# Kernel optimization log

Measured on AMD Instinct MI355X. Metric: run time of the kernel, lower is better.

The kernel has to match this reference:

```python
import jax, jax.numpy as jnp
import numpy as np

TEMPERATURE = 0.07
SIM_THRESHOLD = 0.5


def setup_inputs() -> dict:
    key = jax.random.key(0)
    k1, k2 = jax.random.split(key)
    features = jax.random.normal(k1, (4096, 2, 128), dtype=jnp.float32)
    labels = jax.random.randint(k2, (4096, 100), 0, 2).astype(jnp.float32)
    return {"features": features, "labels": labels}


def reference(features, labels):
    B, V, D = features.shape

    # label Jaccard similarity -> positive/negative masks [B, B]
    intersection = labels @ labels.T
    row_sum = jnp.sum(labels, axis=1, keepdims=True)
    union = row_sum + row_sum.T - intersection
    similarity = intersection / (union + 1e-6)
    positive_mask = (similarity >= SIM_THRESHOLD).astype(jnp.float32)
    negative_mask = 1.0 - positive_mask

    # torch.cat(torch.unbind(features, dim=1), dim=0) -> [V*B, D] (view-major)
    contrast_feature = jnp.transpose(features, (1, 0, 2)).reshape(V * B, D)
    dot_similarities = (contrast_feature @ contrast_feature.T) / TEMPERATURE  # [VB, VB]

    # numerical stability: subtract detached row max over the FULL row
    logits_max = jax.lax.stop_gradient(jnp.max(dot_similarities, axis=1, keepdims=True))
    logits = dot_similarities - logits_max

    # only the top-left [B, B] block is ever indexed by the original loop
    e = jnp.exp(logits[:B, :B])
    pos_sum = jnp.sum(e * positive_mask, axis=1)  # [B]
    neg_sum = jnp.sum(e * negative_mask, axis=1)  # [B]

    has_pos = jnp.sum(positive_mask, axis=1) > 0  # rows with >=1 positive
    pos_safe = jnp.where(has_pos, pos_sum, 1.0)
    den_safe = jnp.where(has_pos, pos_sum + neg_sum, 1.0)
    per_row = -jnp.log(pos_safe / den_safe)

    count = jnp.sum(has_pos.astype(jnp.float32))
    loss = jnp.sum(jnp.where(has_pos, per_row, 0.0)) / jnp.maximum(count, 1.0)
    return loss
```

## Files before the change

### kernel.cpp

```cpp
#include <hip/hip_runtime.h>
#include <math.h>

#define B_ROWS 4096
#define LBL 100
#define NCT 32
#define NTRI 528

typedef __attribute__((ext_vector_type(8))) short bf16x8;
typedef __attribute__((ext_vector_type(4))) float f32x4;

__device__ __forceinline__ unsigned f2bf(float x) {
  union { float f; unsigned u; } a; a.f = x;
  unsigned r = a.u + 0x7fffu + ((a.u >> 16) & 1u);
  return r >> 16;
}
__device__ __forceinline__ float bf2f(unsigned h) {
  return __uint_as_float(h << 16);
}

__global__ void prep_kernel(const float* __restrict__ feat,
                            const float* __restrict__ labels,
                            uint4* __restrict__ cf,
                            uint4* __restrict__ Lb,
                            int* __restrict__ rsv,
                            float* __restrict__ seedRaw,
                            float2* __restrict__ rowAcc,
                            unsigned* __restrict__ counter) {
  if (blockIdx.x == 0 && threadIdx.x == 0) *counter = 0u;
  int w = blockIdx.x * 4 + (threadIdx.x >> 6);
  int lane = threadIdx.x & 63;
  float2 f = ((const float2*)(feat + (size_t)w * 256))[lane];
  unsigned u0 = f2bf(f.x), u1 = f2bf(f.y);
  unsigned myu = u0 | (u1 << 16);
  float b0 = bf2f(u0), b1 = bf2f(u1);
  float s = b0 * b0 + b1 * b1;
  #pragma unroll
  for (int o = 32; o >= 1; o >>= 1) s += __shfl_xor(s, o);
  float x0 = labels[(size_t)w * LBL + lane];
  float x1 = (lane < LBL - 64) ? labels[(size_t)w * LBL + 64 + lane] : 0.0f;
  unsigned long long m0 = __ballot(x0 != 0.0f);
  unsigned long long m1 = __ballot(x1 != 0.0f);
  int kc = lane & 15;
  unsigned q0 = __shfl(myu, kc * 4 + 0);
  unsigned q1 = __shfl(myu, kc * 4 + 1);
  unsigned q2 = __shfl(myu, kc * 4 + 2);
  unsigned q3 = __shfl(myu, kc * 4 + 3);
  if (lane < 16)
    cf[(size_t)(w >> 7) * 2048 + kc * 128 + ((w & 127) ^ kc)] =
        make_uint4(q0, q1, q2, q3);
  if (lane == 0) {
    Lb[w] = make_uint4((unsigned)m0, (unsigned)(m0 >> 32),
                       (unsigned)m1, (unsigned)(m1 >> 32));
    rsv[w] = __popcll(m0) + __popcll(m1);
    seedRaw[w] = s - 0.15f;
    rowAcc[w] = make_float2(0.0f, 0.0f);
  }
}

__launch_bounds__(256, 1)
__global__ void main_kernel(const uint4* __restrict__ cf,
                            const uint4* __restrict__ Lb,
                            const int* __restrict__ rsv,
                            const float* __restrict__ seedRaw,
                            float2* __restrict__ rowAcc,
                            unsigned* __restrict__ counter,
                            float* __restrict__ out) {
  __shared__ unsigned s_done;
  __shared__ float s_p[4], s_c[4];

  int bid = blockIdx.x;
  int bx = 0, off = 0;
  while (bid >= off + (NCT - bx)) { off += NCT - bx; ++bx; }
  int by = bx + (bid - off);
  const bool diag = (bx == by);

  const int tid = threadIdx.x;
  const int lane = tid & 63;
  const int l15 = lane & 15;
  const int quad = lane >> 4;
  const int wave = tid >> 6;
  const int wi = (wave & 1) * 64;
  const int wj = (wave >> 1) * 64;
  const int rowBase = bx * 128;
  const int colBase = by * 128;
  const float invT = 1.0f / 0.07f;

  const uint4* Ab = cf + (size_t)bx * 2048;
  const uint4* Bb = cf + (size_t)by * 2048;

  f32x4 acc[4][4];
  #pragma unroll
  for (int ti = 0; ti < 4; ++ti)
    #pragma unroll
    for (int tj = 0; tj < 4; ++tj)
      acc[ti][tj] = (f32x4){0.f, 0.f, 0.f, 0.f};

  bf16x8 af[4], bfr[4], af2[4], bfr2[4];
  {
    const int kc = quad;
    #pragma unroll
    for (int t = 0; t < 4; ++t) {
      af[t]  = *(const bf16x8*)&Ab[kc * 128 + ((wi + t * 16 + l15) ^ kc)];
      bfr[t] = *(const bf16x8*)&Bb[kc * 128 + ((wj + t * 16 + l15) ^ kc)];
    }
  }
  #pragma unroll
  for (int ks = 0; ks < 4; ++ks) {
    if (ks < 3) {
      const int kc = (ks + 1) * 4 + quad;
      #pragma unroll
      for (int t = 0; t < 4; ++t) {
        af2[t]  = *(const bf16x8*)&Ab[kc * 128 + ((wi + t * 16 + l15) ^ kc)];
        bfr2[t] = *(const bf16x8*)&Bb[kc * 128 + ((wj + t * 16 + l15) ^ kc)];
      }
    }
    #pragma unroll
    for (int ti = 0; ti < 4; ++ti)
      #pragma unroll
      for (int tj = 0; tj < 4; ++tj)
        acc[ti][tj] = __builtin_amdgcn_mfma_f32_16x16x32_bf16(
            af[ti], bfr[tj], acc[ti][tj], 0, 0, 0);
    if (ks < 3) {
      #pragma unroll
      for (int t = 0; t < 4; ++t) { af[t] = af2[t]; bfr[t] = bfr2[t]; }
    }
  }

  uint4 clb[4];
  int crs[4];
  float scol[4], srow[16];
  #pragma unroll
  for (int tj = 0; tj < 4; ++tj) {
    int gcol = colBase + wj + tj * 16 + l15;
    clb[tj] = Lb[gcol];
    crs[tj] = rsv[gcol];
    scol[tj] = seedRaw[gcol];
  }
  #pragma unroll
  for (int ti = 0; ti < 4; ++ti) {
    float4 s4 = *(const float4*)&seedRaw[rowBase + wi + ti * 16 + quad * 4];
    srow[ti * 4 + 0] = s4.x; srow[ti * 4 + 1] = s4.y;
    srow[ti * 4 + 2] = s4.z; srow[ti * 4 + 3] = s4.w;
  }

  float p_s[16], n_s[16], cp[4], cn[4], cmax[4];
  #pragma unroll
  for (int i = 0; i < 16; ++i) { p_s[i] = 0.f; n_s[i] = 0.f; }
  #pragma unroll
  for (int tj = 0; tj < 4; ++tj) { cp[tj] = 0.f; cn[tj] = 0.f; cmax[tj] = -1e30f; }

  #pragma unroll
  for (int ti = 0; ti < 4; ++ti)
    #pragma unroll
    for (int r = 0; r < 4; ++r) {
      int si = ti * 4 + r;
      float l0 = acc[ti][0][r], l1 = acc[ti][1][r];
      float l2 = acc[ti][2][r], l3 = acc[ti][3][r];
      cmax[0] = fmaxf(cmax[0], l0);
      cmax[1] = fmaxf(cmax[1], l1);
      cmax[2] = fmaxf(cmax[2], l2);
      cmax[3] = fmaxf(cmax[3], l3);
      float tm = fmaxf(fmaxf(l0, l1), fmaxf(l2, l3));
      if (tm > srow[si] - 6.3f) {
        int grow = rowBase + wi + ti * 16 + quad * 4 + r;
        uint4 la = Lb[grow];
        int ra = rsv[grow];
        float p = p_s[si], n = n_s[si];
        float lv[4] = {l0, l1, l2, l3};
        #pragma unroll
        for (int tj = 0; tj < 4; ++tj) {
          float e = __expf((lv[tj] - srow[si]) * invT);
          int inter = __popc(la.x & clb[tj].x) + __popc(la.y & clb[tj].y) +
                      __popc(la.z & clb[tj].z) + __popc(la.w & clb[tj].w);
          if (3 * inter > ra + crs[tj]) p += e; else n += e;
        }
        p_s[si] = p;
        n_s[si] = n;
      }
    }

  if (!diag) {
    #pragma unroll
    for (int tj = 0; tj < 4; ++tj) {
      if (cmax[tj] > scol[tj] - 6.3f) {
        float p = cp[tj], n = cn[tj];
        #pragma unroll
        for (int ti = 0; ti < 4; ++ti)
          #pragma unroll
          for (int r = 0; r < 4; ++r) {
            float e = __expf((acc[ti][tj][r] - scol[tj]) * invT);
            int grow = rowBase + wi + ti * 16 + quad * 4 + r;
            uint4 la = Lb[grow];
            int inter = __popc(la.x & clb[tj].x) + __popc(la.y & clb[tj].y) +
                        __popc(la.z & clb[tj].z) + __popc(la.w & clb[tj].w);
            if (3 * inter > rsv[grow] + crs[tj]) p += e; else n += e;
          }
        cp[tj] = p;
        cn[tj] = n;
      }
    }
  }

  #pragma unroll
  for (int si = 0; si < 16; ++si) {
    float p = p_s[si], n = n_s[si];
    #pragma unroll
    for (int o = 8; o >= 1; o >>= 1) {
      p += __shfl_xor(p, o);
      n += __shfl_xor(n, o);
    }
    p_s[si] = p;
    n_s[si] = n;
  }
  if (l15 == 0) {
    #pragma unroll
    for (int ti = 0; ti < 4; ++ti)
      #pragma unroll
      for (int r = 0; r < 4; ++r) {
        float p = p_s[ti * 4 + r], n = n_s[ti * 4 + r];
        if (p != 0.f || n != 0.f) {
          int row = rowBase + wi + ti * 16 + quad * 4 + r;
          atomicAdd(&rowAcc[row].x, p);
          atomicAdd(&rowAcc[row].y, n);
        }
      }
  }
  #pragma unroll
  for (int tj = 0; tj < 4; ++tj) {
    float p = cp[tj], n = cn[tj];
    p += __shfl_xor(p, 16); n += __shfl_xor(n, 16);
    p += __shfl_xor(p, 32); n += __shfl_xor(n, 32);
    cp[tj] = p;
    cn[tj] = n;
  }
  if (!diag && quad == 0) {
    #pragma unroll
    for (int tj = 0; tj < 4; ++tj) {
      if (cp[tj] != 0.f || cn[tj] != 0.f) {
        int col = colBase + wj + tj * 16 + l15;
        atomicAdd(&rowAcc[col].x, cp[tj]);
        atomicAdd(&rowAcc[col].y, cn[tj]);
      }
    }
  }

  asm volatile("s_waitcnt vmcnt(0)" ::: "memory");
  __syncthreads();
  if (tid == 0) s_done = atomicAdd(counter, 1u);
  __syncthreads();
  if (s_done == NTRI - 1) {
    float per = 0.f, cnt = 0.f;
    #pragma unroll
    for (int it = 0; it < B_ROWS / 256; ++it) {
      int row = it * 256 + tid;
      unsigned long long u = __hip_atomic_load(
          (const unsigned long long*)&rowAcc[row], __ATOMIC_RELAXED,
          __HIP_MEMORY_SCOPE_AGENT);
      float p = __uint_as_float((unsigned)u);
      float n = __uint_as_float((unsigned)(u >> 32));
      if (rsv[row] > 0) {
        per += -logf(p / (p + n));
        cnt += 1.f;
      }
    }
    #pragma unroll
    for (int o = 32; o >= 1; o >>= 1) {
      per += __shfl_xor(per, o);
      cnt += __shfl_xor(cnt, o);
    }
    if ((tid & 63) == 0) { s_p[tid >> 6] = per; s_c[tid >> 6] = cnt; }
    __syncthreads();
    if (tid == 0) {
      float P = s_p[0] + s_p[1] + s_p[2] + s_p[3];
      float C = s_c[0] + s_c[1] + s_c[2] + s_c[3];
      out[0] = P / fmaxf(C, 1.0f);
    }
  }
}

extern "C" void kernel_launch(void* const* d_in, const int* in_sizes, int n_in,
                              void* d_out, int out_size, void* d_ws, size_t ws_size,
                              hipStream_t stream) {
  const float* feat = (const float*)d_in[0];
  const float* labels = (const float*)d_in[1];
  float* out = (float*)d_out;
  char* ws = (char*)d_ws;
  uint4* cf = (uint4*)(ws + 0);
  uint4* Lbm = (uint4*)(ws + 1048576);
  int* rsv = (int*)(ws + 1114112);
  float* seedRaw = (float*)(ws + 1130496);
  float2* rowAcc = (float2*)(ws + 1146880);
  unsigned* counter = (unsigned*)(ws + 1146880 + 32768);

  hipLaunchKernelGGL(prep_kernel, dim3(1024), dim3(256), 0, stream,
                     feat, labels, cf, Lbm, rsv, seedRaw, rowAcc, counter);
  hipLaunchKernelGGL(main_kernel, dim3(NTRI), dim3(256), 0, stream,
                     cf, Lbm, rsv, seedRaw, rowAcc, counter, out);
}
```

Measured before the change: 84.13 us.

## Make main kernel persistent with three tiles per block and cross-tile prefetch

Launches 176 blocks that each process three triangular 128x128 tiles in sequence, instead of 528 blocks with one tile each. The first K-chunk of the next tile's operands is prefetched during the last MFMA step of the current tile, and the completion counter threshold is adjusted to match. This is meant to cut launch and tail overhead and to hide load latency across tiles. The cost is fewer blocks than the 256 CUs, so some CUs sit idle, and the larger unrolled body may raise register pressure.

```diff
diff --git a/kernel.cpp b/kernel.cpp
--- a/kernel.cpp
+++ b/kernel.cpp
@@ -5,6 +5,8 @@
 #define LBL 100
 #define NCT 32
 #define NTRI 528
+#define NBLK 176
+#define TPB 3
 
 typedef __attribute__((ext_vector_type(8))) short bf16x8;
 typedef __attribute__((ext_vector_type(4))) float f32x4;
@@ -68,12 +70,6 @@
   __shared__ unsigned s_done;
   __shared__ float s_p[4], s_c[4];
 
-  int bid = blockIdx.x;
-  int bx = 0, off = 0;
-  while (bid >= off + (NCT - bx)) { off += NCT - bx; ++bx; }
-  int by = bx + (bid - off);
-  const bool diag = (bx == by);
-
   const int tid = threadIdx.x;
   const int lane = tid & 63;
   const int l15 = lane & 15;
@@ -81,22 +77,22 @@
   const int wave = tid >> 6;
   const int wi = (wave & 1) * 64;
   const int wj = (wave >> 1) * 64;
-  const int rowBase = bx * 128;
-  const int colBase = by * 128;
   const float invT = 1.0f / 0.07f;
 
-  const uint4* Ab = cf + (size_t)bx * 2048;
-  const uint4* Bb = cf + (size_t)by * 2048;
-
-  f32x4 acc[4][4];
+  int bxA[TPB], byA[TPB];
   #pragma unroll
-  for (int ti = 0; ti < 4; ++ti)
-    #pragma unroll
-    for (int tj = 0; tj < 4; ++tj)
-      acc[ti][tj] = (f32x4){0.f, 0.f, 0.f, 0.f};
+  for (int tt = 0; tt < TPB; ++tt) {
+    int bid = blockIdx.x + tt * NBLK;
+    int bx = 0, off = 0;
+    while (bid >= off + (NCT - bx)) { off += NCT - bx; ++bx; }
+    bxA[tt] = bx;
+    byA[tt] = bx + (bid - off);
+  }
 
   bf16x8 af[4], bfr[4], af2[4], bfr2[4];
   {
+    const uint4* Ab = cf + (size_t)bxA[0] * 2048;
+    const uint4* Bb = cf + (size_t)byA[0] * 2048;
     const int kc = quad;
     #pragma unroll
     for (int t = 0; t < 4; ++t) {
@@ -104,142 +100,169 @@
       bfr[t] = *(const bf16x8*)&Bb[kc * 128 + ((wj + t * 16 + l15) ^ kc)];
     }
   }
+
   #pragma unroll
-  for (int ks = 0; ks < 4; ++ks) {
-    if (ks < 3) {
-      const int kc = (ks + 1) * 4 + quad;
-      #pragma unroll
-      for (int t = 0; t < 4; ++t) {
-        af2[t]  = *(const bf16x8*)&Ab[kc * 128 + ((wi + t * 16 + l15) ^ kc)];
-        bfr2[t] = *(const bf16x8*)&Bb[kc * 128 + ((wj + t * 16 + l15) ^ kc)];
-      }
-    }
+  for (int tt = 0; tt < TPB; ++tt) {
+    const int bx = bxA[tt], by = byA[tt];
+    const bool diag = (bx == by);
+    const int rowBase = bx * 128;
+    const int colBase = by * 128;
+    const uint4* Ab = cf + (size_t)bx * 2048;
+    const uint4* Bb = cf + (size_t)by * 2048;
+
+    uint4 clb[4];
+    int crs[4];
+    float scol[4], srow[16];
+    #pragma unroll
+    for (int tj = 0; tj < 4; ++tj) {
+      int gcol = colBase + wj + tj * 16 + l15;
+      clb[tj] = Lb[gcol];
+      crs[tj] = rsv[gcol];
+      scol[tj] = seedRaw[gcol];
+    }
+    #pragma unroll
+    for (int ti = 0; ti < 4; ++ti) {
+      float4 s4 = *(const float4*)&seedRaw[rowBase + wi + ti * 16 + quad * 4];
+      srow[ti * 4 + 0] = s4.x; srow[ti * 4 + 1] = s4.y;
+      srow[ti * 4 + 2] = s4.z; srow[ti * 4 + 3] = s4.w;
+    }
+
+    f32x4 acc[4][4];
     #pragma unroll
     for (int ti = 0; ti < 4; ++ti)
       #pragma unroll
       for (int tj = 0; tj < 4; ++tj)
-        acc[ti][tj] = __builtin_amdgcn_mfma_f32_16x16x32_bf16(
-            af[ti], bfr[tj], acc[ti][tj], 0, 0, 0);
-    if (ks < 3) {
-      #pragma unroll
-      for (int t = 0; t < 4; ++t) { af[t] = af2[t]; bfr[t] = bfr2[t]; }
-    }
-  }
-
-  uint4 clb[4];
-  int crs[4];
-  float scol[4], srow[16];
-  #pragma unroll
-  for (int tj = 0; tj < 4; ++tj) {
-    int gcol = colBase + wj + tj * 16 + l15;
-    clb[tj] = Lb[gcol];
-    crs[tj] = rsv[gcol];
-    scol[tj] = seedRaw[gcol];
-  }
-  #pragma unroll
-  for (int ti = 0; ti < 4; ++ti) {
-    float4 s4 = *(const float4*)&seedRaw[rowBase + wi + ti * 16 + quad * 4];
-    srow[ti * 4 + 0] = s4.x; srow[ti * 4 + 1] = s4.y;
-    srow[ti * 4 + 2] = s4.z; srow[ti * 4 + 3] = s4.w;
-  }
-
-  float p_s[16], n_s[16], cp[4], cn[4], cmax[4];
-  #pragma unroll
-  for (int i = 0; i < 16; ++i) { p_s[i] = 0.f; n_s[i] = 0.f; }
-  #pragma unroll
-  for (int tj = 0; tj < 4; ++tj) { cp[tj] = 0.f; cn[tj] = 0.f; cmax[tj] = -1e30f; }
-
-  #pragma unroll
-  for (int ti = 0; ti < 4; ++ti)
-    #pragma unroll
-    for (int r = 0; r < 4; ++r) {
-      int si = ti * 4 + r;
-      float l0 = acc[ti][0][r], l1 = acc[ti][1][r];
-      float l2 = acc[ti][2][r], l3 = acc[ti][3][r];
-      cmax[0] = fmaxf(cmax[0], l0);
-      cmax[1] = fmaxf(cmax[1], l1);
-      cmax[2] = fmaxf(cmax[2], l2);
-      cmax[3] = fmaxf(cmax[3], l3);
-      float tm = fmaxf(fmaxf(l0, l1), fmaxf(l2, l3));
-      if (tm > srow[si] - 6.3f) {
-        int grow = rowBase + wi + ti * 16 + quad * 4 + r;
-        uint4 la = Lb[grow];
-        int ra = rsv[grow];
-        float p = p_s[si], n = n_s[si];
-        float lv[4] = {l0, l1, l2, l3};
-        #pragma unroll
-        for (int tj = 0; tj < 4; ++tj) {
-          float e = __expf((lv[tj] - srow[si]) * invT);
-          int inter = __popc(la.x & clb[tj].x) + __popc(la.y & clb[tj].y) +
-                      __popc(la.z & clb[tj].z) + __popc(la.w & clb[tj].w);
-          if (3 * inter > ra + crs[tj]) p += e; else n += e;
-        }
-        p_s[si] = p;
-        n_s[si] = n;
-      }
-    }
-
-  if (!diag) {
-    #pragma unroll
-    for (int tj = 0; tj < 4; ++tj) {
-      if (cmax[tj] > scol[tj] - 6.3f) {
-        float p = cp[tj], n = cn[tj];
-        #pragma unroll
-        for (int ti = 0; ti < 4; ++ti)
+        acc[ti][tj] = (f32x4){0.f, 0.f, 0.f, 0.f};
+
+    #pragma unroll
+    for (int ks = 0; ks < 4; ++ks) {
+      if (ks < 3) {
+        const int kc = (ks + 1) * 4 + quad;
+        #pragma unroll
+        for (int t = 0; t < 4; ++t) {
+          af2[t]  = *(const bf16x8*)&Ab[kc * 128 + ((wi + t * 16 + l15) ^ kc)];
+          bfr2[t] = *(const bf16x8*)&Bb[kc * 128 + ((wj + t * 16 + l15) ^ kc)];
+        }
+      } else if (tt < TPB - 1) {
+        const uint4* An = cf + (size_t)bxA[tt + 1] * 2048;
+        const uint4* Bn = cf + (size_t)byA[tt + 1] * 2048;
+        const int kc = quad;
+        #pragma unroll
+        for (int t = 0; t < 4; ++t) {
+          af2[t]  = *(const bf16x8*)&An[kc * 128 + ((wi + t * 16 + l15) ^ kc)];
+          bfr2[t] = *(const bf16x8*)&Bn[kc * 128 + ((wj + t * 16 + l15) ^ kc)];
+        }
+      }
+      #pragma unroll
+      for (int ti = 0; ti < 4; ++ti)
+        #pragma unroll
+        for (int tj = 0; tj < 4; ++tj)
+          acc[ti][tj] = __builtin_amdgcn_mfma_f32_16x16x32_bf16(
+              af[ti], bfr[tj], acc[ti][tj], 0, 0, 0);
+      if (ks < 3 || tt < TPB - 1) {
+        #pragma unroll
+        for (int t = 0; t < 4; ++t) { af[t] = af2[t]; bfr[t] = bfr2[t]; }
+      }
+    }
+
+    float p_s[16], n_s[16], cp[4], cn[4], cmax[4];
+    #pragma unroll
+    for (int i = 0; i < 16; ++i) { p_s[i] = 0.f; n_s[i] = 0.f; }
+    #pragma unroll
+    for (int tj = 0; tj < 4; ++tj) { cp[tj] = 0.f; cn[tj] = 0.f; cmax[tj] = -1e30f; }
+
+    #pragma unroll
+    for (int ti = 0; ti < 4; ++ti)
+      #pragma unroll
+      for (int r = 0; r < 4; ++r) {
+        int si = ti * 4 + r;
+        float l0 = acc[ti][0][r], l1 = acc[ti][1][r];
+        float l2 = acc[ti][2][r], l3 = acc[ti][3][r];
+        cmax[0] = fmaxf(cmax[0], l0);
+        cmax[1] = fmaxf(cmax[1], l1);
+        cmax[2] = fmaxf(cmax[2], l2);
+        cmax[3] = fmaxf(cmax[3], l3);
+        float tm = fmaxf(fmaxf(l0, l1), fmaxf(l2, l3));
+        if (tm > srow[si] - 6.3f) {
+          int grow = rowBase + wi + ti * 16 + quad * 4 + r;
+          uint4 la = Lb[grow];
+          int ra = rsv[grow];
+          float p = p_s[si], n = n_s[si];
+          float lv[4] = {l0, l1, l2, l3};
           #pragma unroll
-          for (int r = 0; r < 4; ++r) {
-            float e = __expf((acc[ti][tj][r] - scol[tj]) * invT);
-            int grow = rowBase + wi + ti * 16 + quad * 4 + r;
-            uint4 la = Lb[grow];
+          for (int tj = 0; tj < 4; ++tj) {
+            float e = __expf((lv[tj] - srow[si]) * invT);
             int inter = __popc(la.x & clb[tj].x) + __popc(la.y & clb[tj].y) +
                         __popc(la.z & clb[tj].z) + __popc(la.w & clb[tj].w);
-            if (3 * inter > rsv[grow] + crs[tj]) p += e; else n += e;
+            if (3 * inter > ra + crs[tj]) p += e; else n += e;
           }
-        cp[tj] = p;
-        cn[tj] = n;
-      }
-    }
-  }
-
-  #pragma unroll
-  for (int si = 0; si < 16; ++si) {
-    float p = p_s[si], n = n_s[si];
-    #pragma unroll
-    for (int o = 8; o >= 1; o >>= 1) {
-      p += __shfl_xor(p, o);
-      n += __shfl_xor(n, o);
-    }
-    p_s[si] = p;
-    n_s[si] = n;
-  }
-  if (l15 == 0) {
-    #pragma unroll
-    for (int ti = 0; ti < 4; ++ti)
-      #pragma unroll
-      for (int r = 0; r < 4; ++r) {
-        float p = p_s[ti * 4 + r], n = n_s[ti * 4 + r];
-        if (p != 0.f || n != 0.f) {
-          int row = rowBase + wi + ti * 16 + quad * 4 + r;
-          atomicAdd(&rowAcc[row].x, p);
-          atomicAdd(&rowAcc[row].y, n);
-        }
-      }
-  }
-  #pragma unroll
-  for (int tj = 0; tj < 4; ++tj) {
-    float p = cp[tj], n = cn[tj];
-    p += __shfl_xor(p, 16); n += __shfl_xor(n, 16);
-    p += __shfl_xor(p, 32); n += __shfl_xor(n, 32);
-    cp[tj] = p;
-    cn[tj] = n;
-  }
-  if (!diag && quad == 0) {
+          p_s[si] = p;
+          n_s[si] = n;
+        }
+      }
+
+    if (!diag) {
+      #pragma unroll
+      for (int tj = 0; tj < 4; ++tj) {
+        if (cmax[tj] > scol[tj] - 6.3f) {
+          float p = cp[tj], n = cn[tj];
+          #pragma unroll
+          for (int ti = 0; ti < 4; ++ti)
+            #pragma unroll
+            for (int r = 0; r < 4; ++r) {
+              float e = __expf((acc[ti][tj][r] - scol[tj]) * invT);
+              int grow = rowBase + wi + ti * 16 + quad * 4 + r;
+              uint4 la = Lb[grow];
+              int inter = __popc(la.x & clb[tj].x) + __popc(la.y & clb[tj].y) +
+                          __popc(la.z & clb[tj].z) + __popc(la.w & clb[tj].w);
+              if (3 * inter > rsv[grow] + crs[tj]) p += e; else n += e;
+            }
+          cp[tj] = p;
+          cn[tj] = n;
+        }
+      }
+    }
+
+    #pragma unroll
+    for (int si = 0; si < 16; ++si) {
+      float p = p_s[si], n = n_s[si];
+      #pragma unroll
+      for (int o = 8; o >= 1; o >>= 1) {
+        p += __shfl_xor(p, o);
+        n += __shfl_xor(n, o);
+      }
+      p_s[si] = p;
+      n_s[si] = n;
+    }
+    if (l15 == 0) {
+      #pragma unroll
+      for (int ti = 0; ti < 4; ++ti)
+        #pragma unroll
+        for (int r = 0; r < 4; ++r) {
+          float p = p_s[ti * 4 + r], n = n_s[ti * 4 + r];
+          if (p != 0.f || n != 0.f) {
+            int row = rowBase + wi + ti * 16 + quad * 4 + r;
+            atomicAdd(&rowAcc[row].x, p);
+            atomicAdd(&rowAcc[row].y, n);
+          }
+        }
+    }
     #pragma unroll
     for (int tj = 0; tj < 4; ++tj) {
-      if (cp[tj] != 0.f || cn[tj] != 0.f) {
-        int col = colBase + wj + tj * 16 + l15;
-        atomicAdd(&rowAcc[col].x, cp[tj]);
-        atomicAdd(&rowAcc[col].y, cn[tj]);
+      float p = cp[tj], n = cn[tj];
+      p += __shfl_xor(p, 16); n += __shfl_xor(n, 16);
+      p += __shfl_xor(p, 32); n += __shfl_xor(n, 32);
+      cp[tj] = p;
+      cn[tj] = n;
+    }
+    if (!diag && quad == 0) {
+      #pragma unroll
+      for (int tj = 0; tj < 4; ++tj) {
+        if (cp[tj] != 0.f || cn[tj] != 0.f) {
+          int col = colBase + wj + tj * 16 + l15;
+          atomicAdd(&rowAcc[col].x, cp[tj]);
+          atomicAdd(&rowAcc[col].y, cn[tj]);
+        }
       }
     }
   }
@@ -248,7 +271,7 @@
   __syncthreads();
   if (tid == 0) s_done = atomicAdd(counter, 1u);
   __syncthreads();
-  if (s_done == NTRI - 1) {
+  if (s_done == NBLK - 1) {
     float per = 0.f, cnt = 0.f;
     #pragma unroll
     for (int it = 0; it < B_ROWS / 256; ++it) {
@@ -294,6 +317,6 @@
 
   hipLaunchKernelGGL(prep_kernel, dim3(1024), dim3(256), 0, stream,
                      feat, labels, cf, Lbm, rsv, seedRaw, rowAcc, counter);
-  hipLaunchKernelGGL(main_kernel, dim3(NTRI), dim3(256), 0, stream,
+  hipLaunchKernelGGL(main_kernel, dim3(NBLK), dim3(256), 0, stream,
                      cf, Lbm, rsv, seedRaw, rowAcc, counter, out);
 }
```

Measured after the change: 83.54 us. No clear change (-0.7%).
